# Kernel optimization log

Hardware: AMD Instinct MI355X
Metric: run time of the kernel (lower is better)

The kernel has to match this reference:

```python
import jax, jax.numpy as jnp
import numpy as np
from jax import lax

THRESHOLD = 0.5  # score threshold from __init__
IOU_THRESH = 0.5  # batched_nms iou threshold
IMG_W = 1333
IMG_H = 800
NUM_CLASSES = 91
N = 4096  # candidates per view


def _make_boxes(key, n, w, h):
    k1, k2, k3, k4 = jax.random.split(key, 4)
    cx = jax.random.uniform(k1, (n,), minval=0.0, maxval=float(w))
    cy = jax.random.uniform(k2, (n,), minval=0.0, maxval=float(h))
    bw = jax.random.uniform(k3, (n,), minval=4.0, maxval=200.0)
    bh = jax.random.uniform(k4, (n,), minval=4.0, maxval=200.0)
    x1 = jnp.clip(cx - bw / 2, 0.0, float(w))
    x2 = jnp.clip(cx + bw / 2, 0.0, float(w))
    y1 = jnp.clip(cy - bh / 2, 0.0, float(h))
    y2 = jnp.clip(cy + bh / 2, 0.0, float(h))
    return jnp.stack([x1, y1, x2, y2], axis=1).astype(jnp.float32)


def setup_inputs() -> dict:
    key = jax.random.key(0)
    ks = jax.random.split(key, 6)
    return {
        'boxes1': _make_boxes(ks[0], N, IMG_W, IMG_H),
        'boxes2': _make_boxes(ks[1], N, IMG_W, IMG_H),
        'scores1': jax.random.uniform(ks[2], (N,), dtype=jnp.float32),
        'scores2': jax.random.uniform(ks[3], (N,), dtype=jnp.float32),
        'labels1': jax.random.randint(ks[4], (N,), 0, NUM_CLASSES, dtype=jnp.int32),
        'labels2': jax.random.randint(ks[5], (N,), 0, NUM_CLASSES, dtype=jnp.int32),
        'width': IMG_W,
    }


def _pairwise_iou(b):
    # b: [M,4] xyxy -> [M,M] IoU
    area = (b[:, 2] - b[:, 0]) * (b[:, 3] - b[:, 1])
    lt = jnp.maximum(b[:, None, :2], b[None, :, :2])
    rb = jnp.minimum(b[:, None, 2:], b[None, :, 2:])
    wh = jnp.clip(rb - lt, 0.0)
    inter = wh[..., 0] * wh[..., 1]
    return inter / (area[:, None] + area[None, :] - inter + 1e-9)


def reference(boxes1, boxes2, scores1, scores2, labels1, labels2, width):
    w = jnp.asarray(width, dtype=boxes2.dtype)
    # undo hflip on view 2: x1' = width - x2, x2' = width - x1
    b2 = jnp.stack([w - boxes2[:, 2], boxes2[:, 1], w - boxes2[:, 0], boxes2[:, 3]], axis=1)
    boxes = jnp.concatenate([boxes1, b2], axis=0)        # [2N,4]
    scores = jnp.concatenate([scores1, scores2], axis=0)  # [2N]
    labels = jnp.concatenate([labels1, labels2], axis=0)  # [2N]

    # score threshold -> mark invalid instead of dynamic slicing
    valid = scores >= THRESHOLD
    s = jnp.where(valid, scores, -1.0)

    M = boxes.shape[0]
    order = jnp.argsort(-s)  # descending by score
    sb = boxes[order]
    sl = labels[order]
    sv = valid[order]

    # batched_nms via per-class coordinate offset (torchvision trick)
    max_coord = jnp.max(boxes) + 1.0
    ob = sb + (sl.astype(sb.dtype) * max_coord)[:, None]
    iou = _pairwise_iou(ob)  # [2N,2N], the dominant memory traffic

    idx = jnp.arange(M)

    def body(active, i):
        keep_i = active[i]
        suppress = keep_i & (iou[i] > IOU_THRESH) & (idx > i)
        return active & ~suppress, keep_i

    _, keeps = lax.scan(body, sv, idx)  # keeps[i]: box at sorted pos i survives

    boxes_out = jnp.where(keeps[:, None], sb, 0.0)
    scores_out = jnp.where(keeps, scores[order], 0.0)
    labels_out = jnp.where(keeps, sl, -1)
    return boxes_out, labels_out, scores_out, keeps
```

## Files before the change

### kernel.cpp

```cpp
#include <hip/hip_runtime.h>
#include <stdint.h>

typedef unsigned long long u64;

#define NCAND   4096
#define M2      8192
#define NCLS    91
#define SCORE_T 0.5f
#define IOU_T   0.5f
#define JSPLIT  16
#define MAXMEMB 512

#define OFF_HDR     0
#define OFF_KEYS    4096
#define OFF_PART    (OFF_KEYS + 65536)
#define OFF_OAREA   (OFF_PART + JSPLIT*32768)
#define OFF_SSCORE  (OFF_OAREA + 32768)
#define OFF_SLABEL  (OFF_SSCORE + 32768)
#define OFF_SB      (OFF_SLABEL + 32768)
#define OFF_OBOX    (OFF_SB + 131072)

__device__ __forceinline__ unsigned order_key(float f) {
    unsigned u = __float_as_uint(f);
    return (u & 0x80000000u) ? ~u : (u | 0x80000000u);
}

__device__ __forceinline__ float get_width(const int* widthp) {
    int wi = widthp[0];
    return (wi > 0 && wi < 1000000) ? (float)wi : __int_as_float(wi);
}

__device__ __forceinline__ float iou5(float4 a, float aa, float4 b, float ba) {
#pragma clang fp contract(off)
    float ltx = fmaxf(a.x, b.x);
    float lty = fmaxf(a.y, b.y);
    float rbx = fminf(a.z, b.z);
    float rby = fminf(a.w, b.w);
    float wx = fmaxf(rbx - ltx, 0.0f);
    float wy = fmaxf(rby - lty, 0.0f);
    float inter = wx * wy;
    return inter / (((aa + ba) - inter) + 1e-9f);
}

__device__ __forceinline__ void fetch_cand(int idx, const float* b1, const float* b2,
                                           const float* s1, const float* s2,
                                           const int* l1, const int* l2, float wf,
                                           float& x1, float& y1, float& x2, float& y2,
                                           float& sc, int& lb) {
#pragma clang fp contract(off)
    if (idx < NCAND) {
        x1 = b1[idx*4+0]; y1 = b1[idx*4+1]; x2 = b1[idx*4+2]; y2 = b1[idx*4+3];
        sc = s1[idx]; lb = l1[idx];
    } else {
        int m = idx - NCAND;
        float bx1 = b2[m*4+0], by1 = b2[m*4+1], bx2 = b2[m*4+2], by2 = b2[m*4+3];
        x1 = wf - bx2; y1 = by1; x2 = wf - bx1; y2 = by2;
        sc = s2[m]; lb = l2[m];
    }
}

extern "C" __global__ __launch_bounds__(512)
void k_build(const float* __restrict__ b1, const float* __restrict__ b2,
             const float* __restrict__ s1, const float* __restrict__ s2,
             const int* __restrict__ l1, const int* __restrict__ l2,
             const int* __restrict__ widthp, char* __restrict__ ws)
{
#pragma clang fp contract(off)
    const int e = blockIdx.x * 512 + threadIdx.x;
    const float wf = get_width(widthp);
    float x1, y1, x2, y2, sc; int lb;
    fetch_cand(e, b1, b2, s1, s2, l1, l2, wf, x1, y1, x2, y2, sc, lb);

    float lmax = fmaxf(fmaxf(x1, y1), fmaxf(x2, y2));
    for (int d = 32; d > 0; d >>= 1) lmax = fmaxf(lmax, __shfl_xor(lmax, d));
    if ((threadIdx.x & 63) == 0)
        atomicMax(((int*)(ws + OFF_HDR)) + 1, __float_as_int(lmax));

    bool valid = sc >= SCORE_T;
    float s = valid ? sc : -1.0f;
    u64 key = ((u64)order_key(-s) << 32) | (unsigned)e;
    ((u64*)(ws + OFF_KEYS))[e] = key;
}

extern "C" __global__ __launch_bounds__(256)
void k_count(char* __restrict__ ws)
{
    __shared__ u64 tile[M2 / JSPLIT];
    const u64* keys = (const u64*)(ws + OFF_KEYS);
    const int i = blockIdx.x * 256 + threadIdx.x;
    const u64 mykey = keys[i];
    const int j0 = blockIdx.y * (M2 / JSPLIT);
    for (int q = threadIdx.x; q < M2 / JSPLIT; q += 256) tile[q] = keys[j0 + q];
    __syncthreads();
    int cnt = 0;
#pragma unroll 8
    for (int q = 0; q < M2 / JSPLIT; ++q) cnt += (tile[q] < mykey) ? 1 : 0;
    ((int*)(ws + OFF_PART))[blockIdx.y * M2 + i] = cnt;
}

extern "C" __global__ __launch_bounds__(1024)
void k_scatter(const float* __restrict__ b1, const float* __restrict__ b2,
               const float* __restrict__ s1, const float* __restrict__ s2,
               const int* __restrict__ l1, const int* __restrict__ l2,
               const int* __restrict__ widthp, char* __restrict__ ws)
{
#pragma clang fp contract(off)
    const int i = blockIdx.x * 1024 + threadIdx.x;
    const int* part = (const int*)(ws + OFF_PART);
    int rank = 0;
#pragma unroll
    for (int sp = 0; sp < JSPLIT; ++sp) rank += part[sp * M2 + i];

    const float wf = get_width(widthp);
    const float maxc = __int_as_float(((const int*)(ws + OFF_HDR))[1]) + 1.0f;
    float x1, y1, x2, y2, sc; int lb;
    fetch_cand(i, b1, b2, s1, s2, l1, l2, wf, x1, y1, x2, y2, sc, lb);

    float off = (float)lb * maxc;
    float ox1 = x1 + off, oy1 = y1 + off, ox2 = x2 + off, oy2 = y2 + off;
    float area = (ox2 - ox1) * (oy2 - oy1);

    ((float4*)(ws + OFF_SB))[rank]   = make_float4(x1, y1, x2, y2);
    ((float4*)(ws + OFF_OBOX))[rank] = make_float4(ox1, oy1, ox2, oy2);
    ((float*)(ws + OFF_OAREA))[rank]  = area;
    ((float*)(ws + OFF_SSCORE))[rank] = sc;
    ((int*)(ws + OFF_SLABEL))[rank]   = lb;

    bool valid = sc >= SCORE_T;
    u64 bal = __ballot(valid);
    int vmax = valid ? rank + 1 : INT32_MIN;
    for (int d = 32; d > 0; d >>= 1) vmax = max(vmax, __shfl_xor(vmax, d));
    if ((threadIdx.x & 63) == 0 && bal)
        atomicMax((int*)(ws + OFF_HDR), vmax);
}

extern "C" __global__ __launch_bounds__(256)
void k_classnms(const char* __restrict__ ws, float* __restrict__ out)
{
#pragma clang fp contract(off)
    __shared__ unsigned short memb[4][MAXMEMB];
    __shared__ float4 cbox[4][64];
    __shared__ float  carea[4][64];
    __shared__ u64    kmask[4][MAXMEMB / 64];

    const int tid = threadIdx.x;
    const int g = tid >> 6, lane = tid & 63;
    const int wid = blockIdx.x * 4 + g;
    int V = ((const int*)(ws + OFF_HDR))[0];
    if (V < 0) V = 0; if (V > M2) V = M2;

    const int*    slabel = (const int*)   (ws + OFF_SLABEL);
    const float4* obox   = (const float4*)(ws + OFF_OBOX);
    const float*  oarea  = (const float*) (ws + OFF_OAREA);
    const float4* sb     = (const float4*)(ws + OFF_SB);
    const float*  sscore = (const float*) (ws + OFF_SSCORE);

    for (int p = V + wid * 64 + lane; p < M2; p += 96 * 64) {
        ((float4*)out)[p] = make_float4(0.f, 0.f, 0.f, 0.f);
        out[M2*4 + p] = -1.0f;
        out[M2*5 + p] = 0.0f;
        out[M2*6 + p] = 0.0f;
    }
    if (wid >= NCLS) return;
    const int c = wid;

    int n = 0;
    for (int p0 = 0; p0 < V; p0 += 256) {
        int pA = p0 + lane, pB = p0 + 64 + lane, pC = p0 + 128 + lane, pD = p0 + 192 + lane;
        int lA = (pA < V) ? slabel[pA] : -1;
        int lB = (pB < V) ? slabel[pB] : -1;
        int lC = (pC < V) ? slabel[pC] : -1;
        int lD = (pD < V) ? slabel[pD] : -1;
        const u64 lt = (1ull << lane) - 1;
        u64 bal;
        bal = __ballot(lA == c);
        if (lA == c) { int q = n + __popcll(bal & lt); if (q < MAXMEMB) memb[g][q] = (unsigned short)pA; }
        n += __popcll(bal);
        bal = __ballot(lB == c);
        if (lB == c) { int q = n + __popcll(bal & lt); if (q < MAXMEMB) memb[g][q] = (unsigned short)pB; }
        n += __popcll(bal);
        bal = __ballot(lC == c);
        if (lC == c) { int q = n + __popcll(bal & lt); if (q < MAXMEMB) memb[g][q] = (unsigned short)pC; }
        n += __popcll(bal);
        bal = __ballot(lD == c);
        if (lD == c) { int q = n + __popcll(bal & lt); if (q < MAXMEMB) memb[g][q] = (unsigned short)pD; }
        n += __popcll(bal);
    }
    if (n > MAXMEMB) n = MAXMEMB;

    for (int t = 0; t * 64 < n; ++t) {
        int j = t * 64 + lane;
        bool have = j < n;
        int p = have ? (int)memb[g][j] : 0;
        float4 mb = make_float4(0.f, 0.f, 0.f, 0.f);
        float ma = 0.f;
        if (have) { mb = obox[p]; ma = oarea[p]; }
        cbox[g][lane] = mb;
        carea[g][lane] = ma;

        bool supp = false;
        for (int tt = 0; tt < t; ++tt) {
            u64 kb = kmask[g][tt];
            while (kb) {
                int jj = __ffsll(kb) - 1; kb &= kb - 1;
                int pp = (int)memb[g][tt * 64 + jj];
                float4 ob = obox[pp];
                float  oa = oarea[pp];
                supp = supp || (iou5(mb, ma, ob, oa) > IOU_T);
            }
        }

        u64 diag = 0;
        int lim = n - t * 64; if (lim > 64) lim = 64;
        for (int jj = 0; jj < lim; ++jj) {
            float4 ob = cbox[g][jj];
            float  oa = carea[g][jj];
            if (have && jj < lane && (iou5(mb, ma, ob, oa) > IOU_T)) diag |= 1ull << jj;
        }

        bool live = have && !supp;
        u64 k = __ballot(live);
        for (int it = 0; it < 64; ++it) {
            bool killed = (diag & k) != 0;
            u64 k2 = __ballot(live && !killed);
            if (k2 == k) break;
            k = k2;
        }
        if (lane == 0) kmask[g][t] = k;

        if (have) {
            bool kept = (k >> lane) & 1ull;
            float4 bx = kept ? sb[p] : make_float4(0.f, 0.f, 0.f, 0.f);
            ((float4*)out)[p] = bx;
            out[M2*4 + p] = kept ? (float)c : -1.0f;
            out[M2*5 + p] = kept ? sscore[p] : 0.0f;
            out[M2*6 + p] = kept ? 1.0f : 0.0f;
        }
    }
}

extern "C" void kernel_launch(void* const* d_in, const int* in_sizes, int n_in,
                              void* d_out, int out_size, void* d_ws, size_t ws_size,
                              hipStream_t stream)
{
    const float* boxes1  = (const float*)d_in[0];
    const float* boxes2  = (const float*)d_in[1];
    const float* scores1 = (const float*)d_in[2];
    const float* scores2 = (const float*)d_in[3];
    const int*   labels1 = (const int*)d_in[4];
    const int*   labels2 = (const int*)d_in[5];
    const int*   widthp  = (const int*)d_in[6];
    char* ws = (char*)d_ws;

    hipLaunchKernelGGL(k_build, dim3(M2 / 512), dim3(512), 0, stream,
                       boxes1, boxes2, scores1, scores2, labels1, labels2, widthp, ws);
    hipLaunchKernelGGL(k_count, dim3(M2 / 256, JSPLIT), dim3(256), 0, stream, ws);
    hipLaunchKernelGGL(k_scatter, dim3(M2 / 1024), dim3(1024), 0, stream,
                       boxes1, boxes2, scores1, scores2, labels1, labels2, widthp, ws);
    hipLaunchKernelGGL(k_classnms, dim3(24), dim3(256), 0, stream, ws, (float*)d_out);
}
```

Baseline: 116.5 us.

## Fuse key build into rank-count kernel and skip invalid candidates

Removes the separate key-building kernel. The counting kernel now computes sort keys directly from the inputs for its own element and its shared-memory tile, and also performs the max-coordinate reduction in the first y-slice. Counting and scattering are now done only for candidates above the score threshold, relying on invalid keys sorting after all valid ones. This saves a launch and a global key round-trip, at the cost of redundant input fetches per tile, and it leaves invalid sorted slots unwritten.

New measurement: 113.6 us. 1.03x faster.

```diff
diff --git a/kernel.cpp b/kernel.cpp
--- a/kernel.cpp
+++ b/kernel.cpp
@@ -12,8 +12,7 @@
 #define MAXMEMB 512
 
 #define OFF_HDR     0
-#define OFF_KEYS    4096
-#define OFF_PART    (OFF_KEYS + 65536)
+#define OFF_PART    4096
 #define OFF_OAREA   (OFF_PART + JSPLIT*32768)
 #define OFF_SSCORE  (OFF_OAREA + 32768)
 #define OFF_SLABEL  (OFF_SSCORE + 32768)
@@ -59,43 +58,49 @@
     }
 }
 
-extern "C" __global__ __launch_bounds__(512)
-void k_build(const float* __restrict__ b1, const float* __restrict__ b2,
-             const float* __restrict__ s1, const float* __restrict__ s2,
-             const int* __restrict__ l1, const int* __restrict__ l2,
-             const int* __restrict__ widthp, char* __restrict__ ws)
-{
-#pragma clang fp contract(off)
-    const int e = blockIdx.x * 512 + threadIdx.x;
-    const float wf = get_width(widthp);
-    float x1, y1, x2, y2, sc; int lb;
-    fetch_cand(e, b1, b2, s1, s2, l1, l2, wf, x1, y1, x2, y2, sc, lb);
-
-    float lmax = fmaxf(fmaxf(x1, y1), fmaxf(x2, y2));
-    for (int d = 32; d > 0; d >>= 1) lmax = fmaxf(lmax, __shfl_xor(lmax, d));
-    if ((threadIdx.x & 63) == 0)
-        atomicMax(((int*)(ws + OFF_HDR)) + 1, __float_as_int(lmax));
-
+__device__ __forceinline__ u64 make_key(float sc, int e) {
     bool valid = sc >= SCORE_T;
     float s = valid ? sc : -1.0f;
-    u64 key = ((u64)order_key(-s) << 32) | (unsigned)e;
-    ((u64*)(ws + OFF_KEYS))[e] = key;
+    return ((u64)order_key(-s) << 32) | (unsigned)e;
 }
 
 extern "C" __global__ __launch_bounds__(256)
-void k_count(char* __restrict__ ws)
-{
+void k_count2(const float* __restrict__ b1, const float* __restrict__ b2,
+              const float* __restrict__ s1, const float* __restrict__ s2,
+              const int* __restrict__ l1, const int* __restrict__ l2,
+              const int* __restrict__ widthp, char* __restrict__ ws)
+{
+#pragma clang fp contract(off)
     __shared__ u64 tile[M2 / JSPLIT];
-    const u64* keys = (const u64*)(ws + OFF_KEYS);
-    const int i = blockIdx.x * 256 + threadIdx.x;
-    const u64 mykey = keys[i];
+    const int tid = threadIdx.x;
+    const int i = blockIdx.x * 256 + tid;
+    const float wf = get_width(widthp);
+
+    float x1, y1, x2, y2, sc; int lb;
+    fetch_cand(i, b1, b2, s1, s2, l1, l2, wf, x1, y1, x2, y2, sc, lb);
+    const u64 mykey = make_key(sc, i);
+    const bool valid = sc >= SCORE_T;
+    if (blockIdx.y == 0) {
+        float lmax = fmaxf(fmaxf(x1, y1), fmaxf(x2, y2));
+        for (int d = 32; d > 0; d >>= 1) lmax = fmaxf(lmax, __shfl_xor(lmax, d));
+        if ((tid & 63) == 0)
+            atomicMax(((int*)(ws + OFF_HDR)) + 1, __float_as_int(lmax));
+    }
+
     const int j0 = blockIdx.y * (M2 / JSPLIT);
-    for (int q = threadIdx.x; q < M2 / JSPLIT; q += 256) tile[q] = keys[j0 + q];
+    for (int q = tid; q < M2 / JSPLIT; q += 256) {
+        float tx1, ty1, tx2, ty2, tsc; int tlb;
+        fetch_cand(j0 + q, b1, b2, s1, s2, l1, l2, wf, tx1, ty1, tx2, ty2, tsc, tlb);
+        tile[q] = make_key(tsc, j0 + q);
+    }
     __syncthreads();
-    int cnt = 0;
+
+    if (valid) {
+        int cnt = 0;
 #pragma unroll 8
-    for (int q = 0; q < M2 / JSPLIT; ++q) cnt += (tile[q] < mykey) ? 1 : 0;
-    ((int*)(ws + OFF_PART))[blockIdx.y * M2 + i] = cnt;
+        for (int q = 0; q < M2 / JSPLIT; ++q) cnt += (tile[q] < mykey) ? 1 : 0;
+        ((int*)(ws + OFF_PART))[blockIdx.y * M2 + i] = cnt;
+    }
 }
 
 extern "C" __global__ __launch_bounds__(1024)
@@ -106,27 +111,29 @@
 {
 #pragma clang fp contract(off)
     const int i = blockIdx.x * 1024 + threadIdx.x;
-    const int* part = (const int*)(ws + OFF_PART);
-    int rank = 0;
-#pragma unroll
-    for (int sp = 0; sp < JSPLIT; ++sp) rank += part[sp * M2 + i];
-
     const float wf = get_width(widthp);
-    const float maxc = __int_as_float(((const int*)(ws + OFF_HDR))[1]) + 1.0f;
     float x1, y1, x2, y2, sc; int lb;
     fetch_cand(i, b1, b2, s1, s2, l1, l2, wf, x1, y1, x2, y2, sc, lb);
-
-    float off = (float)lb * maxc;
-    float ox1 = x1 + off, oy1 = y1 + off, ox2 = x2 + off, oy2 = y2 + off;
-    float area = (ox2 - ox1) * (oy2 - oy1);
-
-    ((float4*)(ws + OFF_SB))[rank]   = make_float4(x1, y1, x2, y2);
-    ((float4*)(ws + OFF_OBOX))[rank] = make_float4(ox1, oy1, ox2, oy2);
-    ((float*)(ws + OFF_OAREA))[rank]  = area;
-    ((float*)(ws + OFF_SSCORE))[rank] = sc;
-    ((int*)(ws + OFF_SLABEL))[rank]   = lb;
-
-    bool valid = sc >= SCORE_T;
+    const bool valid = sc >= SCORE_T;
+
+    int rank = 0;
+    if (valid) {
+        const int* part = (const int*)(ws + OFF_PART);
+#pragma unroll
+        for (int sp = 0; sp < JSPLIT; ++sp) rank += part[sp * M2 + i];
+
+        const float maxc = __int_as_float(((const int*)(ws + OFF_HDR))[1]) + 1.0f;
+        float off = (float)lb * maxc;
+        float ox1 = x1 + off, oy1 = y1 + off, ox2 = x2 + off, oy2 = y2 + off;
+        float area = (ox2 - ox1) * (oy2 - oy1);
+
+        ((float4*)(ws + OFF_SB))[rank]   = make_float4(x1, y1, x2, y2);
+        ((float4*)(ws + OFF_OBOX))[rank] = make_float4(ox1, oy1, ox2, oy2);
+        ((float*)(ws + OFF_OAREA))[rank]  = area;
+        ((float*)(ws + OFF_SSCORE))[rank] = sc;
+        ((int*)(ws + OFF_SLABEL))[rank]   = lb;
+    }
+
     u64 bal = __ballot(valid);
     int vmax = valid ? rank + 1 : INT32_MIN;
     for (int d = 32; d > 0; d >>= 1) vmax = max(vmax, __shfl_xor(vmax, d));
@@ -252,9 +259,8 @@
     const int*   widthp  = (const int*)d_in[6];
     char* ws = (char*)d_ws;
 
-    hipLaunchKernelGGL(k_build, dim3(M2 / 512), dim3(512), 0, stream,
+    hipLaunchKernelGGL(k_count2, dim3(M2 / 256, JSPLIT), dim3(256), 0, stream,
                        boxes1, boxes2, scores1, scores2, labels1, labels2, widthp, ws);
-    hipLaunchKernelGGL(k_count, dim3(M2 / 256, JSPLIT), dim3(256), 0, stream, ws);
     hipLaunchKernelGGL(k_scatter, dim3(M2 / 1024), dim3(1024), 0, stream,
                        boxes1, boxes2, scores1, scores2, labels1, labels2, widthp, ws);
     hipLaunchKernelGGL(k_classnms, dim3(24), dim3(256), 0, stream, ws, (float*)d_out);
```
